# Performance work log

Measured on AMD Instinct MI355X. Metric: run time of the kernel, lower is better.

The kernel has to match this reference:

```python
import jax, jax.numpy as jnp
import numpy as np

EPS = 1e-8  # torch F.cosine_similarity eps


def setup_inputs() -> dict:
    key = jax.random.key(0)
    k1, k2, k3, k4 = jax.random.split(key, 4)
    B, N, D = 16384, 4096, 1024
    return {
        "query": jax.random.normal(k1, (B, D), dtype=jnp.float32),
        "prompt_components": 0.02 * jax.random.normal(k2, (N, D), dtype=jnp.float32),
        "component_keys": 0.02 * jax.random.normal(k3, (N, D), dtype=jnp.float32),
        "component_attention": 0.02 * jax.random.normal(k4, (N, D), dtype=jnp.float32),
        "top_k": 8,
    }


def reference(query, prompt_components, component_keys, component_attention, top_k):
    # attended query: elementwise scale by mean attention vector
    attn_mean = component_attention.mean(axis=0)            # [D]
    aq = query * attn_mean                                   # [B, D]

    # cosine similarity vs detached keys (vectorized over all components)
    keys = jax.lax.stop_gradient(component_keys)             # detach, as in torch
    aq_n = aq / jnp.maximum(jnp.linalg.norm(aq, axis=1, keepdims=True), EPS)
    k_n = keys / jnp.maximum(jnp.linalg.norm(keys, axis=1, keepdims=True), EPS)
    sims = aq_n @ k_n.T                                      # [B, N]

    top_values, top_indices = jax.lax.top_k(sims, top_k)     # [B, K]
    weights = jax.nn.softmax(top_values, axis=1)             # [B, K]

    # weighted gather-combine of prompt components
    gathered = prompt_components[top_indices]                # [B, K, D]
    selected_prompts = jnp.einsum("bk,bkd->bd", weights, gathered)  # [B, D]
    selected_keys = component_keys[top_indices]              # [B, K, D]

    return selected_prompts[:, None, :], top_indices, selected_keys
```

## Files before the change

kernel.cpp:

```cpp
#include <hip/hip_runtime.h>
#include <math.h>

#define D_DIM 1024
#define N_COMP 4096
#define B_ROWS 16384
#define TOPK 8
#define NC_Q 16
#define NCAND 64
#define EPSV 1e-8f

typedef __bf16 bf16x8 __attribute__((ext_vector_type(8)));
typedef float f32x4 __attribute__((ext_vector_type(4)));

#define WS_MEAN  0
#define WS_KNORM 1024
#define WS_KNN   5120
#define WS_KN16  4199424
#define WS_CI    6296576
#define WS_TW    7345152
#define WS_TI    7476224

__device__ __forceinline__ unsigned short bf16rne(float f) {
    unsigned int u = __float_as_uint(f);
    return (unsigned short)((u + 0x7FFFu + ((u >> 16) & 1u)) >> 16);
}

__device__ __forceinline__ void gload16(const void* g, void* l) {
    __builtin_amdgcn_global_load_lds(
        (const __attribute__((address_space(1))) void*)g,
        (__attribute__((address_space(3))) void*)l, 16, 0, 0);
}

__device__ __forceinline__ void nt_store4(const float4& v, float* p) {
    f32x4 x;
    x[0] = v.x; x[1] = v.y; x[2] = v.z; x[3] = v.w;
    __builtin_nontemporal_store(x, (f32x4*)p);
}

__global__ void seqmean_kernel(const float* __restrict__ attn,
                               float* __restrict__ mean) {
    __shared__ float tile[128][65];
    const int tid = threadIdx.x;
    const int d0 = blockIdx.x * 64;
    const int c = tid & 63, r0 = tid >> 6;
    float acc = 0.f;
    for (int chunk = 0; chunk < 32; ++chunk) {
        const int base = chunk * 128;
        __syncthreads();
        #pragma unroll
        for (int rr = 0; rr < 32; ++rr) {
            int r = r0 * 32 + rr;
            tile[r][c] = attn[(size_t)(base + r) * D_DIM + d0 + c];
        }
        __syncthreads();
        if (tid < 64) {
            #pragma unroll 8
            for (int r = 0; r < 128; ++r)
                acc = __fadd_rn(acc, tile[r][tid]);
        }
    }
    if (tid < 64) mean[d0 + tid] = __fdiv_rn(acc, (float)N_COMP);
}

__global__ void knorm_kernel(const float* __restrict__ keys,
                             float* __restrict__ knorm) {
    const int wave = threadIdx.x >> 6, lane = threadIdx.x & 63;
    const int n = blockIdx.x * 4 + wave;
    const float* x = keys + (size_t)n * D_DIM;
    const int l = lane & 15, g = lane >> 4;
    float lv0, lv1;
    {
        const float* xx = x + g * 128;
        float p[8];
        #pragma unroll
        for (int j = 0; j < 8; ++j) {
            float e = xx[16 * j + l];
            p[j] = __fmul_rn(e, e);
        }
        float t0 = __fadd_rn(p[0], p[1]), t1 = __fadd_rn(p[2], p[3]);
        float t2 = __fadd_rn(p[4], p[5]), t3 = __fadd_rn(p[6], p[7]);
        lv0 = __fadd_rn(__fadd_rn(t0, t1), __fadd_rn(t2, t3));
    }
    {
        const float* xx = x + (g + 4) * 128;
        float p[8];
        #pragma unroll
        for (int j = 0; j < 8; ++j) {
            float e = xx[16 * j + l];
            p[j] = __fmul_rn(e, e);
        }
        float t0 = __fadd_rn(p[0], p[1]), t1 = __fadd_rn(p[2], p[3]);
        float t2 = __fadd_rn(p[4], p[5]), t3 = __fadd_rn(p[6], p[7]);
        lv1 = __fadd_rn(__fadd_rn(t0, t1), __fadd_rn(t2, t3));
    }
    #pragma unroll
    for (int off = 8; off >= 1; off >>= 1) {
        lv0 = __fadd_rn(lv0, __shfl_down(lv0, off));
        lv1 = __fadd_rn(lv1, __shfl_down(lv1, off));
    }
    float L0 = __shfl(lv0, 0),  L1 = __shfl(lv0, 16),
          L2 = __shfl(lv0, 32), L3 = __shfl(lv0, 48);
    float L4 = __shfl(lv1, 0),  L5 = __shfl(lv1, 16),
          L6 = __shfl(lv1, 32), L7 = __shfl(lv1, 48);
    if (lane == 0) {
        float nk = __fadd_rn(
            __fadd_rn(__fadd_rn(L0, L1), __fadd_rn(L2, L3)),
            __fadd_rn(__fadd_rn(L4, L5), __fadd_rn(L6, L7)));
        knorm[n] = fmaxf(__fsqrt_rn(nk), EPSV);
    }
}

__global__ void knn_kernel(const float* __restrict__ keys,
                           const float* __restrict__ knorm,
                           float* __restrict__ knn,
                           unsigned short* __restrict__ kn16) {
    int n = blockIdx.x;
    float kn = knorm[n];
    int d = threadIdx.x * 4;
    const float* row = keys + (size_t)n * D_DIM + d;
    float* orow = knn + (size_t)n * D_DIM + d;
    unsigned short* o16 = kn16 + (size_t)n * D_DIM + d;
    float r0 = __fdiv_rn(row[0], kn);
    float r1 = __fdiv_rn(row[1], kn);
    float r2 = __fdiv_rn(row[2], kn);
    float r3 = __fdiv_rn(row[3], kn);
    orow[0] = r0; orow[1] = r1; orow[2] = r2; orow[3] = r3;
    o16[0] = bf16rne(r0); o16[1] = bf16rne(r1);
    o16[2] = bf16rne(r2); o16[3] = bf16rne(r3);
}

__global__ void aq16_kernel(const float* __restrict__ q,
                            const float* __restrict__ mean,
                            unsigned short* __restrict__ aq16) {
    size_t i = ((size_t)blockIdx.x * 256 + threadIdx.x) * 8;
    int d = (int)(i & (D_DIM - 1));
    float4 a0 = *(const float4*)(q + i);
    float4 a1 = *(const float4*)(q + i + 4);
    float4 m0 = *(const float4*)(mean + d);
    float4 m1 = *(const float4*)(mean + d + 4);
    uint4 pk;
    pk.x = (unsigned)bf16rne(a0.x * m0.x) | ((unsigned)bf16rne(a0.y * m0.y) << 16);
    pk.y = (unsigned)bf16rne(a0.z * m0.z) | ((unsigned)bf16rne(a0.w * m0.w) << 16);
    pk.z = (unsigned)bf16rne(a1.x * m1.x) | ((unsigned)bf16rne(a1.y * m1.y) << 16);
    pk.w = (unsigned)bf16rne(a1.z * m1.z) | ((unsigned)bf16rne(a1.w * m1.w) << 16);
    *(uint4*)(aq16 + i) = pk;
}

__global__ __launch_bounds__(512, 4) void simtop_mfma(
    const unsigned short* __restrict__ aq16,
    const unsigned short* __restrict__ kn16,
    int* __restrict__ candi, float* __restrict__ candv) {
    __shared__ __align__(16) char RAW[49152];
    uint4* A4 = (uint4*)RAW;
    uint4* B4 = (uint4*)(RAW + 16384);
    float* SIM = (float*)RAW;
    float* VM  = (float*)RAW;
    int*   IM  = (int*)(RAW + 16384);

    const int tid = threadIdx.x;
    const int lane = tid & 63;
    const int wid = tid >> 6;
    const int wr = wid >> 2, wc = wid & 3;
    const int l15 = lane & 15, l4 = lane >> 4;
    const int rb = blockIdx.x >> 2;
    const int qq = blockIdx.x & 3;
    const int row0 = rb * 128;
    const int colQ = qq * 1024;
    const int srow = tid & 127;
    const int sstripe = (tid >> 7) & 1;

    float v[NC_Q]; int ix[NC_Q];
    #pragma unroll
    for (int s = 0; s < NC_Q; ++s) { v[s] = -1e30f; ix[s] = 0; }

    for (int ct = 0; ct < 4; ++ct) {
        const int col0 = colQ + ct * 256;
        f32x4 acc[4][4];
        #pragma unroll
        for (int i = 0; i < 4; ++i)
            #pragma unroll
            for (int j = 0; j < 4; ++j) {
                acc[i][j][0] = 0.f; acc[i][j][1] = 0.f;
                acc[i][j][2] = 0.f; acc[i][j][3] = 0.f;
            }

        for (int kt = 0; kt < 16; ++kt) {
            const int k0 = kt * 64;
            __syncthreads();
            #pragma unroll
            for (int c = 0; c < 2; ++c) {
                int unit = c * 512 + tid;
                int r = unit >> 3, j = unit & 7;
                gload16(aq16 + (size_t)(row0 + r) * D_DIM + k0 + (j ^ (r & 7)) * 8,
                        (char*)A4 + unit * 16);
            }
            #pragma unroll
            for (int c = 0; c < 4; ++c) {
                int unit = c * 512 + tid;
                int r = unit >> 3, j = unit & 7;
                gload16(kn16 + (size_t)(col0 + r) * D_DIM + k0 + (j ^ (r & 7)) * 8,
                        (char*)B4 + unit * 16);
            }
            __syncthreads();
            #pragma unroll
            for (int kk = 0; kk < 2; ++kk) {
                bf16x8 af[4], bfv[4];
                #pragma unroll
                for (int f = 0; f < 4; ++f) {
                    int rowa = wr * 64 + f * 16 + l15;
                    int slot = kk * 4 + l4;
                    af[f] = __builtin_bit_cast(bf16x8,
                              A4[rowa * 8 + (slot ^ (rowa & 7))]);
                    int rowb = wc * 64 + f * 16 + l15;
                    bfv[f] = __builtin_bit_cast(bf16x8,
                              B4[rowb * 8 + (slot ^ (rowb & 7))]);
                }
                #pragma unroll
                for (int i = 0; i < 4; ++i)
                    #pragma unroll
                    for (int j = 0; j < 4; ++j)
                        acc[i][j] = __builtin_amdgcn_mfma_f32_16x16x32_bf16(
                            af[i], bfv[j], acc[i][j], 0, 0, 0);
            }
        }
        #pragma unroll 1
        for (int p = 0; p < 4; ++p) {
            __syncthreads();
            if (wr == (p >> 1) && (wc >> 1) == (p & 1)) {
                #pragma unroll
                for (int i = 0; i < 4; ++i)
                    #pragma unroll
                    for (int j = 0; j < 4; ++j)
                        #pragma unroll
                        for (int rg = 0; rg < 4; ++rg)
                            SIM[(i * 16 + l4 * 4 + rg) * 129 +
                                (wc & 1) * 64 + j * 16 + l15] = acc[i][j][rg];
            }
            __syncthreads();
            if (tid < 256 && (srow >> 6) == (p >> 1)) {
                const float* rp = SIM + (srow & 63) * 129 + sstripe * 64;
                const int gbase = col0 + (p & 1) * 128 + sstripe * 64;
                #pragma unroll 1
                for (int cc = 0; cc < 64; ++cc) {
                    float cv = rp[cc];
                    if (cv > v[NC_Q - 1]) {
                        v[NC_Q - 1] = cv; ix[NC_Q - 1] = gbase + cc;
                        #pragma unroll
                        for (int s = NC_Q - 1; s > 0; --s)
                            if (v[s] > v[s - 1]) {
                                float tv = v[s]; v[s] = v[s - 1]; v[s - 1] = tv;
                                int ti = ix[s]; ix[s] = ix[s - 1]; ix[s - 1] = ti;
                            }
                    }
                }
            }
        }
    }
    __syncthreads();
    if (tid < 256) {
        #pragma unroll
        for (int s = 0; s < NC_Q; ++s) {
            VM[tid * 16 + s] = v[s];
            IM[tid * 16 + s] = ix[s];
        }
    }
    __syncthreads();
    if (tid < 128) {
        int ia = 0, ib = 0;
        size_t obase = (size_t)(row0 + tid) * NCAND + qq * 16;
        #pragma unroll 1
        for (int s = 0; s < NC_Q; ++s) {
            float va = (ia < 16) ? VM[tid * 16 + ia] : -3e38f;
            float vb = (ib < 16) ? VM[(tid + 128) * 16 + ib] : -3e38f;
            int id; float vv;
            if (va >= vb) { id = IM[tid * 16 + ia]; vv = va; ++ia; }
            else          { id = IM[(tid + 128) * 16 + ib]; vv = vb; ++ib; }
            candi[obase + s] = id;
            candv[obase + s] = vv;
        }
    }
}

__global__ __launch_bounds__(256) void rescore_kernel(
    const float* __restrict__ q, const float* __restrict__ knn,
    const float* __restrict__ mean, const int* __restrict__ candi,
    const float* __restrict__ candv,
    float* __restrict__ topw, int* __restrict__ topi) {
    __shared__ float anbuf[D_DIM];
    __shared__ float vbuf[NCAND];
    __shared__ int ibuf[NCAND];
    __shared__ int selid[NCAND];
    __shared__ float snq;
    __shared__ int m_s;
    const int tid = threadIdx.x;
    const int wave = tid >> 6, lane = tid & 63;
    const int b = blockIdx.x;
    const float* qr = q + (size_t)b * D_DIM;

    if (wave == 0) {
        const int l = lane & 15, g = lane >> 4;
        float lv0, lv1;
        {
            const float* x = qr + g * 128;
            const float* m = mean + g * 128;
            float p[8];
            #pragma unroll
            for (int j = 0; j < 8; ++j) {
                float e = __fmul_rn(x[16 * j + l], m[16 * j + l]);
                p[j] = __fmul_rn(e, e);
            }
            float t0 = __fadd_rn(p[0], p[1]), t1 = __fadd_rn(p[2], p[3]);
            float t2 = __fadd_rn(p[4], p[5]), t3 = __fadd_rn(p[6], p[7]);
            lv0 = __fadd_rn(__fadd_rn(t0, t1), __fadd_rn(t2, t3));
        }
        {
            const float* x = qr + (g + 4) * 128;
            const float* m = mean + (g + 4) * 128;
            float p[8];
            #pragma unroll
            for (int j = 0; j < 8; ++j) {
                float e = __fmul_rn(x[16 * j + l], m[16 * j + l]);
                p[j] = __fmul_rn(e, e);
            }
            float t0 = __fadd_rn(p[0], p[1]), t1 = __fadd_rn(p[2], p[3]);
            float t2 = __fadd_rn(p[4], p[5]), t3 = __fadd_rn(p[6], p[7]);
            lv1 = __fadd_rn(__fadd_rn(t0, t1), __fadd_rn(t2, t3));
        }
        #pragma unroll
        for (int off = 8; off >= 1; off >>= 1) {
            lv0 = __fadd_rn(lv0, __shfl_down(lv0, off));
            lv1 = __fadd_rn(lv1, __shfl_down(lv1, off));
        }
        float L0 = __shfl(lv0, 0),  L1 = __shfl(lv0, 16),
              L2 = __shfl(lv0, 32), L3 = __shfl(lv0, 48);
        float L4 = __shfl(lv1, 0),  L5 = __shfl(lv1, 16),
              L6 = __shfl(lv1, 32), L7 = __shfl(lv1, 48);
        if (lane == 0) {
            float nq = __fadd_rn(
                __fadd_rn(__fadd_rn(L0, L1), __fadd_rn(L2, L3)),
                __fadd_rn(__fadd_rn(L4, L5), __fadd_rn(L6, L7)));
            snq = fmaxf(__fsqrt_rn(nq), EPSV);
        }
    }
    __syncthreads();
    const float nqd = snq;

    {
        int d0 = tid * 4;
        float4 qv = *(const float4*)(qr + d0);
        float4 mv = *(const float4*)(mean + d0);
        anbuf[d0 + 0] = __fdiv_rn(__fmul_rn(qv.x, mv.x), nqd);
        anbuf[d0 + 1] = __fdiv_rn(__fmul_rn(qv.y, mv.y), nqd);
        anbuf[d0 + 2] = __fdiv_rn(__fmul_rn(qv.z, mv.z), nqd);
        anbuf[d0 + 3] = __fdiv_rn(__fmul_rn(qv.w, mv.w), nqd);
    }

    if (wave == 1) {
        float av = candv[(size_t)b * NCAND + lane];
        int aid = candi[(size_t)b * NCAND + lane];
        float t8;
        {
            float vv = av; int vid = aid;
            #pragma unroll
            for (int s = 0; s < TOPK; ++s) {
                float bv = vv; int bid = vid;
                #pragma unroll
                for (int off = 32; off >= 1; off >>= 1) {
                    float ov = __shfl_xor(bv, off);
                    int oid = __shfl_xor(bid, off);
                    if (ov > bv || (ov == bv && oid < bid)) { bv = ov; bid = oid; }
                }
                t8 = bv;
                if (vid == bid) vv = -1e30f;
            }
        }
        float thr = t8 - 0.003f * nqd;
        bool sel = (av >= thr);
        unsigned long long mk = __ballot(sel);
        int pos = __popcll(mk & ((1ull << lane) - 1ull));
        if (sel) selid[pos] = aid;
        if (lane == 0) m_s = (int)__popcll(mk);
    }
    __syncthreads();
    const int m = m_s;

    {
        const int s = tid >> 2, chunk = tid & 3;
        if (s < m) {
            const int id = selid[s];
            const int start = chunk * 320;
            const int n4 = (chunk == 3) ? 16 : 80;
            const float4* k4 = (const float4*)(knn + (size_t)id * D_DIM + start);
            const float4* a4 = (const float4*)(anbuf + start);
            float acc = 0.f;
            #pragma unroll 4
            for (int t = 0; t < n4; ++t) {
                float4 kv = k4[t];
                float4 av4 = a4[t];
                acc = __fmaf_rn(av4.x, kv.x, acc);
                acc = __fmaf_rn(av4.y, kv.y, acc);
                acc = __fmaf_rn(av4.z, kv.z, acc);
                acc = __fmaf_rn(av4.w, kv.w, acc);
            }
            float c2 = __shfl_down(acc, 1);
            float c3 = __shfl_down(acc, 2);
            float c4 = __shfl_down(acc, 3);
            if (chunk == 0) {
                vbuf[s] = __fadd_rn(__fadd_rn(__fadd_rn(acc, c2), c3), c4);
                ibuf[s] = id;
            }
        }
    }
    __syncthreads();

    if (wave == 0) {
        float v = (lane < m) ? vbuf[lane] : -3e38f;
        int id = (lane < m) ? ibuf[lane] : 0x7fffffff;
        float sv[TOPK]; int si[TOPK];
        #pragma unroll
        for (int s = 0; s < TOPK; ++s) {
            float bv = v; int bid = id;
            #pragma unroll
            for (int off = 32; off >= 1; off >>= 1) {
                float ov = __shfl_xor(bv, off);
                int oid = __shfl_xor(bid, off);
                if (ov > bv || (ov == bv && oid < bid)) { bv = ov; bid = oid; }
            }
            sv[s] = bv; si[s] = bid;
            if (id == bid) v = -3e38f;
        }
        if (lane == 0) {
            float mx = sv[0];
            float w[TOPK];
            float ssum = 0.f;
            #pragma unroll
            for (int k = 0; k < TOPK; ++k) { w[k] = expf(sv[k] - mx); ssum += w[k]; }
            float rs = 1.0f / ssum;
            #pragma unroll
            for (int k = 0; k < TOPK; ++k) {
                topw[b * TOPK + k] = w[k] * rs;
                topi[b * TOPK + k] = si[k];
            }
        }
    }
}

__global__ void output_kernel(const float* __restrict__ topw,
                              const int* __restrict__ topi,
                              const float* __restrict__ prompts,
                              const float* __restrict__ keys,
                              float* __restrict__ out) {
    int b = blockIdx.x;
    float w[TOPK];
    int id[TOPK];
    #pragma unroll
    for (int k = 0; k < TOPK; ++k) {
        w[k] = topw[b * TOPK + k];
        id[k] = topi[b * TOPK + k];
    }

    const size_t OFF1 = (size_t)B_ROWS * D_DIM;
    const size_t OFF2 = OFF1 + (size_t)B_ROWS * TOPK;

    if (threadIdx.x < TOPK)
        out[OFF1 + (size_t)b * TOPK + threadIdx.x] = (float)id[threadIdx.x];

    int d0 = threadIdx.x * 4;
    float4 acc; acc.x = acc.y = acc.z = acc.w = 0.f;
    #pragma unroll
    for (int k = 0; k < TOPK; ++k) {
        const float* pr = prompts + (size_t)id[k] * D_DIM + d0;
        float4 pv = *(const float4*)pr;
        acc.x += w[k] * pv.x; acc.y += w[k] * pv.y;
        acc.z += w[k] * pv.z; acc.w += w[k] * pv.w;
        const float* kr = keys + (size_t)id[k] * D_DIM + d0;
        float4 kv = *(const float4*)kr;
        nt_store4(kv, out + OFF2 + ((size_t)b * TOPK + k) * D_DIM + d0);
    }
    nt_store4(acc, out + (size_t)b * D_DIM + d0);
}

extern "C" void kernel_launch(void* const* d_in, const int* in_sizes, int n_in,
                              void* d_out, int out_size, void* d_ws, size_t ws_size,
                              hipStream_t stream) {
    const float* query   = (const float*)d_in[0];
    const float* prompts = (const float*)d_in[1];
    const float* keys    = (const float*)d_in[2];
    const float* attn    = (const float*)d_in[3];
    float* ws = (float*)d_ws;
    float* out = (float*)d_out;

    float* mean  = ws + WS_MEAN;
    float* knorm = ws + WS_KNORM;
    float* knn   = ws + WS_KNN;
    unsigned short* kn16 = (unsigned short*)(ws + WS_KN16);
    int*   candi = (int*)(ws + WS_CI);
    float* topw  = ws + WS_TW;
    int*   topi  = (int*)(ws + WS_TI);
    float* outscratch = out + (size_t)B_ROWS * D_DIM + (size_t)B_ROWS * TOPK;
    unsigned short* aq16 = (unsigned short*)outscratch;
    float* candv = outscratch + 8388608;

    seqmean_kernel<<<16, 256, 0, stream>>>(attn, mean);
    knorm_kernel<<<N_COMP / 4, 256, 0, stream>>>(keys, knorm);
    knn_kernel<<<N_COMP, 256, 0, stream>>>(keys, knorm, knn, kn16);
    aq16_kernel<<<8192, 256, 0, stream>>>(query, mean, aq16);
    simtop_mfma<<<512, 512, 0, stream>>>(aq16, kn16, candi, candv);
    rescore_kernel<<<B_ROWS, 256, 0, stream>>>(query, knn, mean, candi, candv,
                                               topw, topi);
    output_kernel<<<B_ROWS, 256, 0, stream>>>(topw, topi, prompts, keys, out);
}
```

Measured before the change: 906.7 us.

## Fuse rescore with output gather and pack candidate id and score into one word

The rescore kernel now writes the final prompt-weighted sum and key gather itself, which removes the separate output kernel launch and the topw/topi round trip through global memory. Candidate id and a bf16-rounded approximate score are packed into a single 32-bit word, so candidate traffic drops by half and the candv buffer goes away. The lower-precision candidate scores bring a wider rescore threshold (0.004 instead of 0.003), which may send more candidates through exact fp32 rescoring. Running the gather inside the rescore blocks also makes each block longer.

After: 898.9 us, median of 2. About the same (-0.9%).

```diff
diff --git a/kernel.cpp b/kernel.cpp
--- a/kernel.cpp
+++ b/kernel.cpp
@@ -17,8 +17,6 @@
 #define WS_KNN   5120
 #define WS_KN16  4199424
 #define WS_CI    6296576
-#define WS_TW    7345152
-#define WS_TI    7476224
 
 __device__ __forceinline__ unsigned short bf16rne(float f) {
     unsigned int u = __float_as_uint(f);
@@ -149,7 +147,7 @@
 __global__ __launch_bounds__(512, 4) void simtop_mfma(
     const unsigned short* __restrict__ aq16,
     const unsigned short* __restrict__ kn16,
-    int* __restrict__ candi, float* __restrict__ candv) {
+    int* __restrict__ candi) {
     __shared__ __align__(16) char RAW[49152];
     uint4* A4 = (uint4*)RAW;
     uint4* B4 = (uint4*)(RAW + 16384);
@@ -275,23 +273,24 @@
             int id; float vv;
             if (va >= vb) { id = IM[tid * 16 + ia]; vv = va; ++ia; }
             else          { id = IM[(tid + 128) * 16 + ib]; vv = vb; ++ib; }
-            candi[obase + s] = id;
-            candv[obase + s] = vv;
-        }
-    }
-}
-
-__global__ __launch_bounds__(256) void rescore_kernel(
+            candi[obase + s] = (id << 16) | (int)bf16rne(vv);
+        }
+    }
+}
+
+__global__ __launch_bounds__(256) void rescore_output_kernel(
     const float* __restrict__ q, const float* __restrict__ knn,
     const float* __restrict__ mean, const int* __restrict__ candi,
-    const float* __restrict__ candv,
-    float* __restrict__ topw, int* __restrict__ topi) {
+    const float* __restrict__ prompts, const float* __restrict__ keys,
+    float* __restrict__ out) {
     __shared__ float anbuf[D_DIM];
     __shared__ float vbuf[NCAND];
     __shared__ int ibuf[NCAND];
     __shared__ int selid[NCAND];
     __shared__ float snq;
     __shared__ int m_s;
+    __shared__ float sw[TOPK];
+    __shared__ int sid[TOPK];
     const int tid = threadIdx.x;
     const int wave = tid >> 6, lane = tid & 63;
     const int b = blockIdx.x;
@@ -356,8 +355,9 @@
     }
 
     if (wave == 1) {
-        float av = candv[(size_t)b * NCAND + lane];
-        int aid = candi[(size_t)b * NCAND + lane];
+        int pk = candi[(size_t)b * NCAND + lane];
+        int aid = (int)(((unsigned)pk) >> 16);
+        float av = __uint_as_float(((unsigned)pk & 0xFFFFu) << 16);
         float t8;
         {
             float vv = av; int vid = aid;
@@ -374,7 +374,7 @@
                 if (vid == bid) vv = -1e30f;
             }
         }
-        float thr = t8 - 0.003f * nqd;
+        float thr = t8 - 0.004f * nqd;
         bool sel = (av >= thr);
         unsigned long long mk = __ballot(sel);
         int pos = __popcll(mk & ((1ull << lane) - 1ull));
@@ -438,34 +438,28 @@
             float rs = 1.0f / ssum;
             #pragma unroll
             for (int k = 0; k < TOPK; ++k) {
-                topw[b * TOPK + k] = w[k] * rs;
-                topi[b * TOPK + k] = si[k];
-            }
-        }
-    }
-}
-
-__global__ void output_kernel(const float* __restrict__ topw,
-                              const int* __restrict__ topi,
-                              const float* __restrict__ prompts,
-                              const float* __restrict__ keys,
-                              float* __restrict__ out) {
-    int b = blockIdx.x;
+                sw[k] = w[k] * rs;
+                sid[k] = si[k];
+            }
+        }
+    }
+    __syncthreads();
+
     float w[TOPK];
     int id[TOPK];
     #pragma unroll
     for (int k = 0; k < TOPK; ++k) {
-        w[k] = topw[b * TOPK + k];
-        id[k] = topi[b * TOPK + k];
+        w[k] = sw[k];
+        id[k] = sid[k];
     }
 
     const size_t OFF1 = (size_t)B_ROWS * D_DIM;
     const size_t OFF2 = OFF1 + (size_t)B_ROWS * TOPK;
 
-    if (threadIdx.x < TOPK)
-        out[OFF1 + (size_t)b * TOPK + threadIdx.x] = (float)id[threadIdx.x];
-
-    int d0 = threadIdx.x * 4;
+    if (tid < TOPK)
+        out[OFF1 + (size_t)b * TOPK + tid] = (float)id[tid];
+
+    int d0 = tid * 4;
     float4 acc; acc.x = acc.y = acc.z = acc.w = 0.f;
     #pragma unroll
     for (int k = 0; k < TOPK; ++k) {
@@ -495,18 +489,14 @@
     float* knn   = ws + WS_KNN;
     unsigned short* kn16 = (unsigned short*)(ws + WS_KN16);
     int*   candi = (int*)(ws + WS_CI);
-    float* topw  = ws + WS_TW;
-    int*   topi  = (int*)(ws + WS_TI);
     float* outscratch = out + (size_t)B_ROWS * D_DIM + (size_t)B_ROWS * TOPK;
     unsigned short* aq16 = (unsigned short*)outscratch;
-    float* candv = outscratch + 8388608;
 
     seqmean_kernel<<<16, 256, 0, stream>>>(attn, mean);
     knorm_kernel<<<N_COMP / 4, 256, 0, stream>>>(keys, knorm);
     knn_kernel<<<N_COMP, 256, 0, stream>>>(keys, knorm, knn, kn16);
     aq16_kernel<<<8192, 256, 0, stream>>>(query, mean, aq16);
-    simtop_mfma<<<512, 512, 0, stream>>>(aq16, kn16, candi, candv);
-    rescore_kernel<<<B_ROWS, 256, 0, stream>>>(query, knn, mean, candi, candv,
-                                               topw, topi);
-    output_kernel<<<B_ROWS, 256, 0, stream>>>(topw, topi, prompts, keys, out);
-}
+    simtop_mfma<<<512, 512, 0, stream>>>(aq16, kn16, candi);
+    rescore_output_kernel<<<B_ROWS, 256, 0, stream>>>(query, knn, mean, candi,
+                                                      prompts, keys, out);
+}
```
